# Performance work log

Measured on AMD Instinct MI355X. Metric: run time of the kernel, lower is better.

## Reference

```python
import jax, jax.numpy as jnp
import numpy as np

B, C, IMG, P = 32, 3, 224, 16
HID, L, NH, DH, INTER, NCLS = 768, 12, 12, 64, 3072, 1000
GP = IMG // P  # 14 patches per side
S = GP * GP + 1  # 197 tokens
EPS = 1e-5  # torch LayerNorm default


def layer_norm(x, scale, bias):
    mu = jnp.mean(x, axis=-1, keepdims=True)
    var = jnp.mean(jnp.square(x - mu), axis=-1, keepdims=True)
    return (x - mu) * jax.lax.rsqrt(var + EPS) * scale + bias


def setup_inputs() -> dict:
    key = jax.random.key(0)
    ks = jax.random.split(key, 16)
    s = 0.02
    d = {
        "x": jax.random.normal(ks[0], (B, C, IMG, IMG), jnp.float32),
        "conv_w": jax.random.normal(ks[1], (HID, C, P, P), jnp.float32) * s,
        "conv_b": jnp.zeros((HID,), jnp.float32),
        "cls_token": jax.random.normal(ks[2], (1, 1, HID), jnp.float32),
        "pos_emb": jax.random.normal(ks[3], (1, S, HID), jnp.float32) * s,
        "ln1_s": jnp.ones((L, HID), jnp.float32),
        "ln1_b": jnp.zeros((L, HID), jnp.float32),
        "wq": jax.random.normal(ks[4], (L, NH, HID, DH), jnp.float32) * s,
        "bq": jnp.zeros((L, NH, DH), jnp.float32),
        "wk": jax.random.normal(ks[5], (L, NH, HID, DH), jnp.float32) * s,
        "bk": jnp.zeros((L, NH, DH), jnp.float32),
        "wv": jax.random.normal(ks[6], (L, NH, HID, DH), jnp.float32) * s,
        "bv": jnp.zeros((L, NH, DH), jnp.float32),
        "wo": jax.random.normal(ks[7], (L, HID, HID), jnp.float32) * s,
        "bo": jnp.zeros((L, HID), jnp.float32),
        "ln2_s": jnp.ones((L, HID), jnp.float32),
        "ln2_b": jnp.zeros((L, HID), jnp.float32),
        "w1": jax.random.normal(ks[8], (L, HID, INTER), jnp.float32) * s,
        "b1": jnp.zeros((L, INTER), jnp.float32),
        "w2": jax.random.normal(ks[9], (L, INTER, HID), jnp.float32) * s,
        "b2": jnp.zeros((L, HID), jnp.float32),
        "head_w": jax.random.normal(ks[10], (HID, NCLS), jnp.float32) * s,
        "head_b": jnp.zeros((NCLS,), jnp.float32),
    }
    return d


def vit_forward(x, conv_w, conv_b, cls_token, pos_emb, ln1_s, ln1_b,
                wq, bq, wk, bk, wv, bv, wo, bo, ln2_s, ln2_b,
                w1, b1, w2, b2, head_w, head_b):
    # Patch embedding: conv stride=kernel=P  ==  patch extract + matmul
    xp = x.reshape(B, C, GP, P, GP, P)
    h = jnp.einsum('bcipjq,dcpq->bijd', xp, conv_w) + conv_b  # [B,GP,GP,HID]
    h = h.reshape(B, GP * GP, HID)
    h = jnp.concatenate([jnp.broadcast_to(cls_token, (B, 1, HID)), h], axis=1)
    h = h + pos_emb  # [B,S,HID]

    scale = 1.0 / np.sqrt(DH).astype(np.float32)
    for l in range(L):
        # --- multi-head attention (per-head linears expressed as stacked einsum) ---
        hn = layer_norm(h, ln1_s[l], ln1_b[l])
        q = jnp.einsum('bsd,hdk->bhsk', hn, wq[l]) + bq[l][None, :, None, :]
        k = jnp.einsum('bsd,hdk->bhsk', hn, wk[l]) + bk[l][None, :, None, :]
        v = jnp.einsum('bsd,hdk->bhsk', hn, wv[l]) + bv[l][None, :, None, :]
        scores = jnp.einsum('bhsk,bhtk->bhst', q, k) * scale
        probs = jax.nn.softmax(scores, axis=-1)
        att = jnp.einsum('bhst,bhtk->bhsk', probs, v)  # [B,NH,S,DH]
        att = att.transpose(0, 2, 1, 3).reshape(B, S, HID)  # concat heads on last dim
        h = h + att @ wo[l] + bo[l]
        # --- MLP ---
        hn = layer_norm(h, ln2_s[l], ln2_b[l])
        m = jax.nn.gelu(hn @ w1[l] + b1[l], approximate=False)
        h = h + m @ w2[l] + b2[l]

    # classifier on [CLS] token
    return h[:, 0, :] @ head_w + head_b  # [B, NCLS]


def reference(x, conv_w, conv_b, cls_token, pos_emb, ln1_s, ln1_b,
              wq, bq, wk, bk, wv, bv, wo, bo, ln2_s, ln2_b,
              w1, b1, w2, b2, head_w, head_b):
    return vit_forward(x, conv_w, conv_b, cls_token, pos_emb, ln1_s, ln1_b,
                       wq, bq, wk, bk, wv, bv, wo, bo, ln2_s, ln2_b,
                       w1, b1, w2, b2, head_w, head_b)
```

## Files before the change

kernel.cpp:

```cpp
#include <hip/hip_runtime.h>
#include <hip/hip_bf16.h>
#include <math.h>


using bf16 = __hip_bfloat16;
typedef __attribute__((ext_vector_type(8))) short short8;
typedef __attribute__((ext_vector_type(4))) float floatx4;

__device__ __forceinline__ void async_copy16(const bf16* g, bf16* l) {
    __builtin_amdgcn_global_load_lds(
        (const __attribute__((address_space(1))) void*)g,
        (__attribute__((address_space(3))) void*)l, 16, 0, 0);
}

template<int OUT_BF16, int ACT_GELU, int RESID>
__global__ __launch_bounds__(256, 4) void gemm_nt(
    const bf16* __restrict__ A, const bf16* __restrict__ B, void* __restrict__ Cout,
    const float* __restrict__ resid, const float* __restrict__ bias, float scale,
    int M, int N, int K, int lda, int ldb, int ldc,
    int batchInner, long sAi, long sAo, long sBi, long sBo, long sCi, long sCo)
{
    __shared__ __align__(16) bf16 As[128 * 32];
    __shared__ __align__(16) bf16 Bs[128 * 32];

    const int bz = blockIdx.z;
    const int bi = bz % batchInner, bo = bz / batchInner;
    const bf16* Ab = A + (long)bi * sAi + (long)bo * sAo;
    const bf16* Bb = B + (long)bi * sBi + (long)bo * sBo;
    const long coff = (long)bi * sCi + (long)bo * sCo;

    const int tid  = threadIdx.x;
    const int lane = tid & 63;
    const int wave = tid >> 6;
    const int wrow = (wave >> 1) << 6;
    const int wcol = (wave & 1) << 6;
    const int quad = lane >> 4;
    const int l16  = lane & 15;
    const int m0 = blockIdx.y << 7;
    const int n0 = blockIdx.x << 7;

    floatx4 acc[4][4];
#pragma unroll
    for (int i = 0; i < 4; i++)
#pragma unroll
        for (int j = 0; j < 4; j++) acc[i][j] = (floatx4)0.0f;

    const int c0 = wave * 2, c1 = wave * 2 + 1;
    const int rIn = lane >> 2;
    const int seg = (lane & 3) << 3;
    const int rA0 = c0 * 16 + rIn, rA1 = c1 * 16 + rIn;
    const long aOff0 = (long)min(m0 + rA0, M - 1) * lda + seg;
    const long aOff1 = (long)min(m0 + rA1, M - 1) * lda + seg;
    const long bOff0 = (long)min(n0 + rA0, N - 1) * ldb + seg;
    const long bOff1 = (long)min(n0 + rA1, N - 1) * ldb + seg;
    bf16* ldsA0 = &As[c0 * 512];
    bf16* ldsA1 = &As[c1 * 512];
    bf16* ldsB0 = &Bs[c0 * 512];
    bf16* ldsB1 = &Bs[c1 * 512];

    const int kTiles = K >> 5;
    for (int kt = 0; kt < kTiles; ++kt) {
        const long kb = (long)kt << 5;
        async_copy16(Ab + aOff0 + kb, ldsA0);
        async_copy16(Ab + aOff1 + kb, ldsA1);
        async_copy16(Bb + bOff0 + kb, ldsB0);
        async_copy16(Bb + bOff1 + kb, ldsB1);
        __syncthreads();

        short8 af[4], bfr[4];
#pragma unroll
        for (int i = 0; i < 4; i++) {
            af[i]  = *(const short8*)(&As[(wrow + i * 16 + l16) * 32 + quad * 8]);
            bfr[i] = *(const short8*)(&Bs[(wcol + i * 16 + l16) * 32 + quad * 8]);
        }
#pragma unroll
        for (int i = 0; i < 4; i++)
#pragma unroll
            for (int j = 0; j < 4; j++)
                acc[i][j] = __builtin_amdgcn_mfma_f32_16x16x32_bf16(
                    af[i], bfr[j], acc[i][j], 0, 0, 0);
        __syncthreads();
    }

#pragma unroll
    for (int i = 0; i < 4; i++) {
        const int rbase = m0 + wrow + i * 16 + quad * 4;
#pragma unroll
        for (int j = 0; j < 4; j++) {
            const int col = n0 + wcol + j * 16 + l16;
            if (col >= N) continue;
            const float bval = bias ? bias[col] : 0.0f;
#pragma unroll
            for (int r = 0; r < 4; r++) {
                const int row = rbase + r;
                if (row >= M) continue;
                const long idx = coff + (long)row * ldc + col;
                float v = acc[i][j][r] * scale + bval;
                if (RESID)    v += resid[idx];
                if (ACT_GELU) v = 0.5f * v * (1.0f + erff(v * 0.70710678118654752f));
                if (OUT_BF16) ((bf16*)Cout)[idx] = __float2bfloat16(v);
                else          ((float*)Cout)[idx] = v;
            }
        }
    }
}

__global__ __launch_bounds__(256) void transpose_cvt(
    const float* __restrict__ src, bf16* __restrict__ dst, int K, int N,
    int srcLd, int dstLd, int batchInner, long sSi, long sSo, long sDi, long sDo)
{
    __shared__ float t[32][33];
    const int bz = blockIdx.z;
    const int bi = bz % batchInner, bo = bz / batchInner;
    const float* S = src + (long)bi * sSi + (long)bo * sSo;
    bf16* D = dst + (long)bi * sDi + (long)bo * sDo;
    const int k0 = blockIdx.y << 5, n0 = blockIdx.x << 5;
    const int tx = threadIdx.x & 31, ty = threadIdx.x >> 5;
#pragma unroll
    for (int i = 0; i < 32; i += 8) {
        int k = k0 + ty + i, n = n0 + tx;
        if (k < K && n < N) t[ty + i][tx] = S[(long)k * srcLd + n];
    }
    __syncthreads();
#pragma unroll
    for (int i = 0; i < 32; i += 8) {
        int n = n0 + ty + i, k = k0 + tx;
        if (n < N && k < K) D[(long)n * dstLd + k] = __float2bfloat16(t[tx][ty + i]);
    }
}

__global__ void cvt_f2b(const float* __restrict__ s, bf16* __restrict__ d, int n) {
    int i = blockIdx.x * 256 + threadIdx.x;
    if (i < n) d[i] = __float2bfloat16(s[i]);
}

__global__ void pack_qkv_bias(const float* __restrict__ bq, const float* __restrict__ bk,
                              const float* __restrict__ bv, float* __restrict__ qb) {
    int i = blockIdx.x * 256 + threadIdx.x;
    int l = i / 2304, n = i % 2304;
    float v = (n < 768) ? bq[l * 768 + n]
            : (n < 1536) ? bk[l * 768 + n - 768]
                         : bv[l * 768 + n - 1536];
    qb[i] = v;
}

__global__ __launch_bounds__(256) void im2col_k(const float* __restrict__ x, bf16* __restrict__ out) {
    const int row = blockIdx.x;
    const int b = row / 196, r = row % 196, gi = r / 14, gj = r % 14;
    const float* xb = x + (long)b * 3 * 224 * 224;
    bf16* o = out + (long)row * 768;
    const int tid = threadIdx.x;
#pragma unroll
    for (int i = 0; i < 3; i++) {
        int col = tid + (i << 8);
        int c = col >> 8, rem = col & 255, p = rem >> 4, q = rem & 15;
        o[col] = __float2bfloat16(xb[((long)c * 224 + gi * 16 + p) * 224 + gj * 16 + q]);
    }
}

__global__ __launch_bounds__(256) void assemble_k(const float* __restrict__ hp,
                                                  const float* __restrict__ cls,
                                                  const float* __restrict__ pos,
                                                  float* __restrict__ h) {
    const int row = blockIdx.x;
    const int b = row / 197, t = row % 197;
    float* o = h + (long)row * 768;
    const float* p = pos + (long)t * 768;
    const int tid = threadIdx.x;
#pragma unroll
    for (int i = 0; i < 3; i++) {
        int c = tid + (i << 8);
        float v = (t == 0) ? cls[c] : hp[((long)(b * 196 + t - 1)) * 768 + c];
        o[c] = v + p[c];
    }
}

__global__ __launch_bounds__(256) void layernorm_k(const float* __restrict__ h,
                                                   const float* __restrict__ gamma,
                                                   const float* __restrict__ beta,
                                                   bf16* __restrict__ out) {
    const int row = blockIdx.x;
    const float* x = h + (long)row * 768;
    const int tid = threadIdx.x;
    float v[3], s = 0.f, ss = 0.f;
#pragma unroll
    for (int i = 0; i < 3; i++) { v[i] = x[tid + (i << 8)]; s += v[i]; ss += v[i] * v[i]; }
#pragma unroll
    for (int o = 32; o; o >>= 1) { s += __shfl_xor(s, o); ss += __shfl_xor(ss, o); }
    __shared__ float red[8];
    const int wave = tid >> 6, lane = tid & 63;
    if (lane == 0) { red[wave] = s; red[4 + wave] = ss; }
    __syncthreads();
    if (tid == 0) {
        red[0] = red[0] + red[1] + red[2] + red[3];
        red[4] = red[4] + red[5] + red[6] + red[7];
    }
    __syncthreads();
    const float mu  = red[0] * (1.0f / 768.0f);
    const float var = red[4] * (1.0f / 768.0f) - mu * mu;
    const float inv = rsqrtf(var + 1e-5f);
    bf16* o = out + (long)row * 768;
#pragma unroll
    for (int i = 0; i < 3; i++) {
        int c = tid + (i << 8);
        o[c] = __float2bfloat16((v[i] - mu) * inv * gamma[c] + beta[c]);
    }
}

__global__ __launch_bounds__(256) void transpose_v(const bf16* __restrict__ qkv,
                                                   bf16* __restrict__ vT) {
    __shared__ bf16 t[64][65];
    const int t0 = blockIdx.x << 6;
    const int bz = blockIdx.y;
    const int b = bz / 12, hh = bz % 12;
    const int tx = threadIdx.x & 63, ty = threadIdx.x >> 6;
#pragma unroll
    for (int i = 0; i < 64; i += 4) {
        int tt = t0 + ty + i;
        bf16 v = __float2bfloat16(0.0f);
        if (tt < 197) v = qkv[((long)(b * 197 + tt)) * 2304 + 1536 + hh * 64 + tx];
        t[ty + i][tx] = v;
    }
    __syncthreads();
    bf16* d = vT + (long)bz * 14336;
#pragma unroll
    for (int i = 0; i < 64; i += 4) {
        int tt = t0 + tx;
        if (tt < 224) d[(long)(ty + i) * 224 + tt] = t[tx][ty + i];
    }
}

__global__ __launch_bounds__(256) void softmax_k(bf16* __restrict__ sc) {
    const int row = blockIdx.x * 4 + (threadIdx.x >> 6);
    const int lane = threadIdx.x & 63;
    bf16* s = sc + (long)row * 224;
    float v0 = __bfloat162float(s[lane]);
    float v1 = __bfloat162float(s[64 + lane]);
    float v2 = __bfloat162float(s[128 + lane]);
    float v3 = (192 + lane < 197) ? __bfloat162float(s[192 + lane]) : -1e30f;
    float m = fmaxf(fmaxf(v0, v1), fmaxf(v2, v3));
#pragma unroll
    for (int o = 32; o; o >>= 1) m = fmaxf(m, __shfl_xor(m, o));
    float e0 = __expf(v0 - m), e1 = __expf(v1 - m), e2 = __expf(v2 - m);
    float e3 = (192 + lane < 197) ? __expf(v3 - m) : 0.0f;
    float t = e0 + e1 + e2 + e3;
#pragma unroll
    for (int o = 32; o; o >>= 1) t += __shfl_xor(t, o);
    const float inv = 1.0f / t;
    s[lane]        = __float2bfloat16(e0 * inv);
    s[64 + lane]   = __float2bfloat16(e1 * inv);
    s[128 + lane]  = __float2bfloat16(e2 * inv);
    if (192 + lane < 224) s[192 + lane] = __float2bfloat16(e3 * inv);
}

__global__ __launch_bounds__(256) void extract_cls(const float* __restrict__ h,
                                                   bf16* __restrict__ hcls) {
    const int b = blockIdx.x, tid = threadIdx.x;
#pragma unroll
    for (int i = 0; i < 3; i++) {
        int c = tid + (i << 8);
        hcls[(long)b * 768 + c] = __float2bfloat16(h[(long)b * 197 * 768 + c]);
    }
}

extern "C" void kernel_launch(void* const* d_in, const int* in_sizes, int n_in,
                              void* d_out, int out_size, void* d_ws, size_t ws_size,
                              hipStream_t stream)
{
    (void)in_sizes; (void)n_in; (void)out_size; (void)ws_size;
    const float* x      = (const float*)d_in[0];
    const float* conv_w = (const float*)d_in[1];
    const float* conv_b = (const float*)d_in[2];
    const float* cls    = (const float*)d_in[3];
    const float* pos    = (const float*)d_in[4];
    const float* ln1_s  = (const float*)d_in[5];
    const float* ln1_b  = (const float*)d_in[6];
    const float* wq     = (const float*)d_in[7];
    const float* bq     = (const float*)d_in[8];
    const float* wk     = (const float*)d_in[9];
    const float* bk     = (const float*)d_in[10];
    const float* wv     = (const float*)d_in[11];
    const float* bv     = (const float*)d_in[12];
    const float* wo     = (const float*)d_in[13];
    const float* bo     = (const float*)d_in[14];
    const float* ln2_s  = (const float*)d_in[15];
    const float* ln2_b  = (const float*)d_in[16];
    const float* w1     = (const float*)d_in[17];
    const float* b1     = (const float*)d_in[18];
    const float* w2     = (const float*)d_in[19];
    const float* b2     = (const float*)d_in[20];
    const float* head_w = (const float*)d_in[21];
    const float* head_b = (const float*)d_in[22];
    float* out = (float*)d_out;

    char* ws = (char*)d_ws;
    size_t off = 0;
    auto take = [&](size_t bytes) -> char* {
        char* p = ws + off; off += (bytes + 255) & ~(size_t)255; return p;
    };
    float* h    = (float*)take(6304UL * 768 * 4);
    bf16*  hn   = (bf16*) take(6304UL * 768 * 2);
    bf16*  qkv  = (bf16*) take(6304UL * 2304 * 2);
    bf16*  att  = (bf16*) take(6304UL * 768 * 2);
    bf16*  Wqkv = (bf16*) take(12UL * 2304 * 768 * 2);
    bf16*  Wo   = (bf16*) take(12UL * 768 * 768 * 2);
    bf16*  W1   = (bf16*) take(12UL * 768 * 3072 * 2);
    bf16*  W2   = (bf16*) take(12UL * 768 * 3072 * 2);
    bf16*  Wp   = (bf16*) take(589824UL * 2);
    bf16*  Wh   = (bf16*) take(768000UL * 2);
    float* qb   = (float*)take(27648UL * 4);
    bf16*  hcls = (bf16*) take(24576UL * 2);
    char*  scr  = take(46UL * 1024 * 1024);
    bf16*  scores = (bf16*)scr;
    bf16*  vT     = (bf16*)(scr + 384UL * 197 * 224 * 2);
    bf16*  inter  = (bf16*)scr;
    bf16*  Apatch = (bf16*)scr;
    float* hpatch = (float*)(scr + ((6272UL * 768 * 2 + 255) & ~(size_t)255));

    cvt_f2b<<<2304, 256, 0, stream>>>(conv_w, Wp, 589824);
    transpose_cvt<<<dim3(2, 24, 144), 256, 0, stream>>>(wq, Wqkv,           768, 64, 64, 768, 12, 49152, 589824, 49152, 1769472);
    transpose_cvt<<<dim3(2, 24, 144), 256, 0, stream>>>(wk, Wqkv + 589824,  768, 64, 64, 768, 12, 49152, 589824, 49152, 1769472);
    transpose_cvt<<<dim3(2, 24, 144), 256, 0, stream>>>(wv, Wqkv + 1179648, 768, 64, 64, 768, 12, 49152, 589824, 49152, 1769472);
    transpose_cvt<<<dim3(24, 24, 12), 256, 0, stream>>>(wo, Wo, 768, 768, 768, 768, 12, 589824, 0, 589824, 0);
    transpose_cvt<<<dim3(96, 24, 12), 256, 0, stream>>>(w1, W1, 768, 3072, 3072, 768, 12, 2359296, 0, 2359296, 0);
    transpose_cvt<<<dim3(24, 96, 12), 256, 0, stream>>>(w2, W2, 3072, 768, 768, 3072, 12, 2359296, 0, 2359296, 0);
    transpose_cvt<<<dim3(32, 24, 1), 256, 0, stream>>>(head_w, Wh, 768, 1000, 1000, 768, 1, 0, 0, 0, 0);
    pack_qkv_bias<<<108, 256, 0, stream>>>(bq, bk, bv, qb);

    im2col_k<<<6272, 256, 0, stream>>>(x, Apatch);
    gemm_nt<0, 0, 0><<<dim3(6, 49, 1), 256, 0, stream>>>(
        Apatch, Wp, hpatch, nullptr, conv_b, 1.0f,
        6272, 768, 768, 768, 768, 768, 1, 0, 0, 0, 0, 0, 0);
    assemble_k<<<6304, 256, 0, stream>>>(hpatch, cls, pos, h);

    for (int l = 0; l < 12; ++l) {
        layernorm_k<<<6304, 256, 0, stream>>>(h, ln1_s + l * 768, ln1_b + l * 768, hn);
        gemm_nt<1, 0, 0><<<dim3(18, 50, 1), 256, 0, stream>>>(
            hn, Wqkv + (size_t)l * 1769472, qkv, nullptr, qb + l * 2304, 1.0f,
            6304, 2304, 768, 768, 768, 2304, 1, 0, 0, 0, 0, 0, 0);
        transpose_v<<<dim3(4, 384), 256, 0, stream>>>(qkv, vT);
        gemm_nt<1, 0, 0><<<dim3(2, 2, 384), 256, 0, stream>>>(
            qkv, qkv + 768, scores, nullptr, nullptr, 0.125f,
            197, 197, 64, 2304, 2304, 224,
            12, 64, 197L * 2304, 64, 197L * 2304, 44128, 529536);
        softmax_k<<<18912, 256, 0, stream>>>(scores);
        gemm_nt<1, 0, 0><<<dim3(1, 2, 384), 256, 0, stream>>>(
            scores, vT, att, nullptr, nullptr, 1.0f,
            197, 64, 224, 224, 224, 768,
            12, 44128, 529536, 14336, 172032, 64, 151296);
        gemm_nt<0, 0, 1><<<dim3(6, 50, 1), 256, 0, stream>>>(
            att, Wo + (size_t)l * 589824, h, h, bo + l * 768, 1.0f,
            6304, 768, 768, 768, 768, 768, 1, 0, 0, 0, 0, 0, 0);
        layernorm_k<<<6304, 256, 0, stream>>>(h, ln2_s + l * 768, ln2_b + l * 768, hn);
        gemm_nt<1, 1, 0><<<dim3(24, 50, 1), 256, 0, stream>>>(
            hn, W1 + (size_t)l * 2359296, inter, nullptr, b1 + l * 3072, 1.0f,
            6304, 3072, 768, 768, 768, 3072, 1, 0, 0, 0, 0, 0, 0);
        gemm_nt<0, 0, 1><<<dim3(6, 50, 1), 256, 0, stream>>>(
            inter, W2 + (size_t)l * 2359296, h, h, b2 + l * 768, 1.0f,
            6304, 768, 3072, 3072, 3072, 768, 1, 0, 0, 0, 0, 0, 0);
    }

    extract_cls<<<32, 256, 0, stream>>>(h, hcls);
    gemm_nt<0, 0, 0><<<dim3(8, 1, 1), 256, 0, stream>>>(
        hcls, Wh, out, nullptr, head_b, 1.0f,
        32, 1000, 768, 768, 768, 1000, 1, 0, 0, 0, 0, 0, 0);
}
```

Measured before the change: 4.677 ms.

## Double-buffer GEMM LDS tiles and remap workgroups across XCDs

Splits the GEMM's LDS staging into two buffers so the async global-to-LDS load of the next K tile is issued before the MFMA work on the current tile. This aims to hide load latency behind compute and drops one barrier per iteration. It also remaps the linear workgroup id so that consecutive tiles land on the same XCD, to improve L2 reuse. The cost is twice the LDS per block, which may lower occupancy.

```diff
diff --git a/kernel.cpp b/kernel.cpp
--- a/kernel.cpp
+++ b/kernel.cpp
@@ -11,6 +11,12 @@
     __builtin_amdgcn_global_load_lds(
         (const __attribute__((address_space(1))) void*)g,
         (__attribute__((address_space(3))) void*)l, 16, 0, 0);
+}
+
+__device__ __forceinline__ void wave_sync_vm0() {
+    asm volatile("s_waitcnt vmcnt(0)" ::: "memory");
+    __builtin_amdgcn_s_barrier();
+    asm volatile("" ::: "memory");
 }
 
 template<int OUT_BF16, int ACT_GELU, int RESID>
@@ -20,14 +26,23 @@
     int M, int N, int K, int lda, int ldb, int ldc,
     int batchInner, long sAi, long sAo, long sBi, long sBo, long sCi, long sCo)
 {
-    __shared__ __align__(16) bf16 As[128 * 32];
-    __shared__ __align__(16) bf16 Bs[128 * 32];
+    __shared__ __align__(16) bf16 As[2][128 * 32];
+    __shared__ __align__(16) bf16 Bs[2][128 * 32];
 
     const int bz = blockIdx.z;
     const int bi = bz % batchInner, bo = bz / batchInner;
     const bf16* Ab = A + (long)bi * sAi + (long)bo * sAo;
     const bf16* Bb = B + (long)bi * sBi + (long)bo * sBo;
     const long coff = (long)bi * sCi + (long)bo * sCo;
+
+    const int nbx = gridDim.x;
+    const int nwg = nbx * gridDim.y;
+    const int orig = blockIdx.y * nbx + blockIdx.x;
+    const int q8 = nwg >> 3, r8 = nwg & 7;
+    const int xcd = orig & 7, sidx = orig >> 3;
+    const int wg = (xcd < r8 ? xcd * (q8 + 1) : r8 * (q8 + 1) + (xcd - r8) * q8) + sidx;
+    const int m0 = (wg / nbx) << 7;
+    const int n0 = (wg % nbx) << 7;
 
     const int tid  = threadIdx.x;
     const int lane = tid & 63;
@@ -36,8 +51,6 @@
     const int wcol = (wave & 1) << 6;
     const int quad = lane >> 4;
     const int l16  = lane & 15;
-    const int m0 = blockIdx.y << 7;
-    const int n0 = blockIdx.x << 7;
 
     floatx4 acc[4][4];
 #pragma unroll
@@ -53,25 +66,21 @@
     const long aOff1 = (long)min(m0 + rA1, M - 1) * lda + seg;
     const long bOff0 = (long)min(n0 + rA0, N - 1) * ldb + seg;
     const long bOff1 = (long)min(n0 + rA1, N - 1) * ldb + seg;
-    bf16* ldsA0 = &As[c0 * 512];
-    bf16* ldsA1 = &As[c1 * 512];
-    bf16* ldsB0 = &Bs[c0 * 512];
-    bf16* ldsB1 = &Bs[c1 * 512];
-
-    const int kTiles = K >> 5;
-    for (int kt = 0; kt < kTiles; ++kt) {
+
+    auto stage = [&](int buf, int kt) {
         const long kb = (long)kt << 5;
-        async_copy16(Ab + aOff0 + kb, ldsA0);
-        async_copy16(Ab + aOff1 + kb, ldsA1);
-        async_copy16(Bb + bOff0 + kb, ldsB0);
-        async_copy16(Bb + bOff1 + kb, ldsB1);
-        __syncthreads();
-
+        async_copy16(Ab + aOff0 + kb, &As[buf][c0 * 512]);
+        async_copy16(Ab + aOff1 + kb, &As[buf][c1 * 512]);
+        async_copy16(Bb + bOff0 + kb, &Bs[buf][c0 * 512]);
+        async_copy16(Bb + bOff1 + kb, &Bs[buf][c1 * 512]);
+    };
+
+    auto compute = [&](const bf16* __restrict__ Asb, const bf16* __restrict__ Bsb) {
         short8 af[4], bfr[4];
 #pragma unroll
         for (int i = 0; i < 4; i++) {
-            af[i]  = *(const short8*)(&As[(wrow + i * 16 + l16) * 32 + quad * 8]);
-            bfr[i] = *(const short8*)(&Bs[(wcol + i * 16 + l16) * 32 + quad * 8]);
+            af[i]  = *(const short8*)(&Asb[(wrow + i * 16 + l16) * 32 + quad * 8]);
+            bfr[i] = *(const short8*)(&Bsb[(wcol + i * 16 + l16) * 32 + quad * 8]);
         }
 #pragma unroll
         for (int i = 0; i < 4; i++)
@@ -79,7 +88,19 @@
             for (int j = 0; j < 4; j++)
                 acc[i][j] = __builtin_amdgcn_mfma_f32_16x16x32_bf16(
                     af[i], bfr[j], acc[i][j], 0, 0, 0);
-        __syncthreads();
+    };
+
+    const int kTiles = K >> 5;
+    stage(0, 0);
+    for (int kt = 0; kt < kTiles; kt += 2) {
+        wave_sync_vm0();
+        if (kt + 1 < kTiles) stage(1, kt + 1);
+        compute(As[0], Bs[0]);
+        if (kt + 1 < kTiles) {
+            wave_sync_vm0();
+            if (kt + 2 < kTiles) stage(0, kt + 2);
+            compute(As[1], Bs[1]);
+        }
     }
 
 #pragma unroll
```

Result: no change. 4.592 ms (-1.8%).
